# Optimization experiments

Hardware: AMD Instinct MI355X
Metric: run time of the kernel (lower is better)

Reference implementation:

```python
import jax, jax.numpy as jnp
import numpy as np
from jax import lax

D_MODEL, D_STATE, D_CONV, D_INNER, DT_RANK = 1024, 16, 4, 2048, 64
B_SZ, L_SEQ = 2, 4096

def setup_inputs() -> dict:
    key = jax.random.key(0)
    ks = jax.random.split(key, 12)
    s = 0.02
    x = jax.random.normal(ks[0], (B_SZ, L_SEQ, D_MODEL), jnp.float32)
    norm_w = jnp.ones((D_MODEL,), jnp.float32)
    norm_b = jnp.zeros((D_MODEL,), jnp.float32)
    W_in = jax.random.normal(ks[1], (D_MODEL, 2 * D_INNER), jnp.float32) * s
    conv_w = jax.random.normal(ks[2], (D_INNER, 1, D_CONV), jnp.float32) * 0.5
    conv_b = jnp.zeros((D_INNER,), jnp.float32)
    W_x = jax.random.normal(ks[3], (D_INNER, DT_RANK + 2 * D_STATE), jnp.float32) * s
    W_dt = jax.random.normal(ks[4], (DT_RANK, D_INNER), jnp.float32) * s
    # dt bias init as in the torch module: inverse-softplus of dt in [dt_min, dt_max]
    dt_init = jnp.exp(jax.random.uniform(ks[5], (D_INNER,)) * (np.log(0.1) - np.log(0.001)) + np.log(0.001))
    dt_init = jnp.clip(dt_init, 1e-4, None)
    b_dt = dt_init + jnp.log(-jnp.expm1(-dt_init))
    A_log = jnp.log(jnp.broadcast_to(jnp.arange(1, D_STATE + 1, dtype=jnp.float32)[None, :], (D_INNER, D_STATE)))
    D = jnp.ones((D_INNER,), jnp.float32)
    W_out = jax.random.normal(ks[6], (D_INNER, D_MODEL), jnp.float32) * s
    return {"x": x, "norm_w": norm_w, "norm_b": norm_b, "W_in": W_in,
            "conv_w": conv_w, "conv_b": conv_b, "W_x": W_x, "W_dt": W_dt,
            "b_dt": b_dt, "A_log": A_log, "D": D, "W_out": W_out}

def _silu(v):
    return v * jax.nn.sigmoid(v)

def _layernorm(v, w, b, eps=1e-5):
    mu = jnp.mean(v, axis=-1, keepdims=True)
    var = jnp.var(v, axis=-1, keepdims=True)
    return (v - mu) * lax.rsqrt(var + eps) * w + b

def _selective_scan(u, delta, A, Bm, Cm, Dp):
    # u, delta: [B,L,d_inner]; A: [d_inner,N]; Bm, Cm: [B,L,N]; Dp: [d_inner]
    Bb, L, d_inner = u.shape
    N = A.shape[1]

    def step(h, inp):
        dt_t, u_t, B_t, C_t = inp  # [B,d_inner],[B,d_inner],[B,N],[B,N]
        A_bar = jnp.exp(dt_t[..., None] * A)                       # [B,d_inner,N]
        h = A_bar * h + dt_t[..., None] * B_t[:, None, :] * u_t[..., None]
        y = jnp.sum(h * C_t[:, None, :], axis=-1)                  # [B,d_inner]
        return h, y

    h0 = jnp.zeros((Bb, d_inner, N), u.dtype)
    xs = (jnp.swapaxes(delta, 0, 1), jnp.swapaxes(u, 0, 1),
          jnp.swapaxes(Bm, 0, 1), jnp.swapaxes(Cm, 0, 1))
    _, ys = lax.scan(step, h0, xs)          # ys: [L,B,d_inner]
    y = jnp.swapaxes(ys, 0, 1)
    return y + u * Dp[None, None, :]

def reference(x, norm_w, norm_b, W_in, conv_w, conv_b, W_x, W_dt, b_dt, A_log, D, W_out):
    residual = x
    xn = _layernorm(x, norm_w, norm_b)
    xz = xn @ W_in                                      # [B,L,2*d_inner]
    x_ssm, z = jnp.split(xz, 2, axis=-1)
    # depthwise causal conv1d (torch pads both sides then truncates -> left pad)
    xt = jnp.swapaxes(x_ssm, 1, 2)                      # [B,d_inner,L]
    xt = jnp.pad(xt, ((0, 0), (0, 0), (D_CONV - 1, 0)))
    xc = lax.conv_general_dilated(xt, conv_w, window_strides=(1,), padding='VALID',
                                  feature_group_count=D_INNER,
                                  dimension_numbers=('NCH', 'OIH', 'NCH'))
    xc = xc + conv_b[None, :, None]
    x_conv = jnp.swapaxes(_silu(xc), 1, 2)              # [B,L,d_inner]
    x_dbl = x_conv @ W_x                                # [B,L,dt_rank+2N]
    dt_low, B_mat, C_mat = jnp.split(x_dbl, [DT_RANK, DT_RANK + D_STATE], axis=-1)
    delta = jax.nn.softplus(dt_low @ W_dt + b_dt)       # [B,L,d_inner]
    A = -jnp.exp(A_log)
    y = _selective_scan(x_conv, delta, A, B_mat, C_mat, D)
    y = y * _silu(z)
    return residual + y @ W_out
```

## Files before the change

### kernel.cpp

```cpp
#include <hip/hip_runtime.h>

typedef unsigned short u16;
typedef __attribute__((ext_vector_type(8))) __bf16 bf16x8;
typedef __attribute__((ext_vector_type(4))) float f32x4;

#define LSEQ 4096
#define DMODEL 1024
#define DINNER 2048

__device__ __forceinline__ float bf2f(u16 u) {
  union { unsigned u; float f; } v; v.u = ((unsigned)u) << 16; return v.f;
}
__device__ __forceinline__ u16 f2bf(float f) {
  union { float f; unsigned u; } v; v.f = f;
  unsigned r = v.u + 0x7fffu + ((v.u >> 16) & 1u);
  return (u16)(r >> 16);
}
__device__ __forceinline__ void gload_lds16(const void* g, void* l) {
  __builtin_amdgcn_global_load_lds(
      (__attribute__((address_space(1))) void*)(unsigned long long)g,
      (__attribute__((address_space(3))) void*)(unsigned int)(unsigned long long)l,
      16, 0, 0);
}
__device__ __forceinline__ float sigmoidf_(float v) { return 1.f / (1.f + __expf(-v)); }

__device__ __forceinline__ void swz_block(int gx, int& bn, int& bm) {
  int lin = blockIdx.x + gridDim.x * blockIdx.y;
  int q = (gridDim.x * gridDim.y) >> 3;
  int s = (lin & 7) * q + (lin >> 3);
  bn = s % gx;
  bm = s / gx;
}

__global__ __launch_bounds__(256) void ln_kernel(const float* __restrict__ x,
                                                 const float* __restrict__ w,
                                                 const float* __restrict__ b,
                                                 u16* __restrict__ out) {
  int row = blockIdx.x;
  const float* xr = x + (size_t)row * DMODEL;
  int t = threadIdx.x;
  float4 v = ((const float4*)xr)[t];
  float s = v.x + v.y + v.z + v.w;
  float s2 = v.x * v.x + v.y * v.y + v.z * v.z + v.w * v.w;
  for (int off = 32; off; off >>= 1) {
    s += __shfl_down(s, off);
    s2 += __shfl_down(s2, off);
  }
  __shared__ float ls[4], ls2[4];
  int wid = t >> 6;
  if ((t & 63) == 0) { ls[wid] = s; ls2[wid] = s2; }
  __syncthreads();
  s = ls[0] + ls[1] + ls[2] + ls[3];
  s2 = ls2[0] + ls2[1] + ls2[2] + ls2[3];
  float mu = s * (1.f / DMODEL);
  float var = s2 * (1.f / DMODEL) - mu * mu;
  float rs = rsqrtf(var + 1e-5f);
  float4 wv = ((const float4*)w)[t];
  float4 bv = ((const float4*)b)[t];
  unsigned p0 = (unsigned)f2bf((v.x - mu) * rs * wv.x + bv.x) |
                ((unsigned)f2bf((v.y - mu) * rs * wv.y + bv.y) << 16);
  unsigned p1 = (unsigned)f2bf((v.z - mu) * rs * wv.z + bv.z) |
                ((unsigned)f2bf((v.w - mu) * rs * wv.w + bv.w) << 16);
  ((uint2*)(out + (size_t)row * DMODEL))[t] = make_uint2(p0, p1);
}

__global__ __launch_bounds__(256) void tc_kernel(const float* __restrict__ in,
                                                 u16* __restrict__ out,
                                                 int K, int N, int Npad) {
  __shared__ float tile[32][33];
  int n0 = blockIdx.x * 32, k0 = blockIdx.y * 32;
  int tx = threadIdx.x & 31, ty = threadIdx.x >> 5;
  for (int i = ty; i < 32; i += 8) {
    int k = k0 + i, n = n0 + tx;
    tile[i][tx] = (k < K && n < N) ? in[(size_t)k * N + n] : 0.f;
  }
  __syncthreads();
  for (int i = ty; i < 32; i += 8) {
    int n = n0 + i, k = k0 + tx;
    if (n < Npad && k < K) out[(size_t)n * K + k] = f2bf(tile[tx][i]);
  }
}

__device__ __forceinline__ void stage8(const u16* grow0, int ld, int kcol0,
                                       u16* lds_u, int ln) {
  int rr = ln >> 3, kb = ln & 7;
  gload_lds16(grow0 + (size_t)rr * ld + kcol0 + ((kb ^ rr) << 3), lds_u);
}

#define LDA_FRAGS(mh, buf)                                                         \
  _Pragma("unroll") for (int mf = 0; mf < 4; ++mf)                                 \
  _Pragma("unroll") for (int kk = 0; kk < 2; ++kk)                                 \
    av[mf][kk] = *(const bf16x8*)(LA + (buf) * 16384 +                             \
        (wm * 128 + (mh) * 64 + mf * 16 + lr) * 64 + (((kk * 4 + lq) ^ key) << 3));

#define LDB_FRAGS(nh, buf)                                                         \
  _Pragma("unroll") for (int nf = 0; nf < 2; ++nf)                                 \
  _Pragma("unroll") for (int kk = 0; kk < 2; ++kk)                                 \
    bb[nh][nf][kk] = *(const bf16x8*)(LB + (buf) * 16384 +                         \
        (wn * 64 + (nh) * 32 + nf * 16 + lr) * 64 + (((kk * 4 + lq) ^ key) << 3));

#define MFMA_Q(mh, nh)                                                             \
  __builtin_amdgcn_s_setprio(1);                                                   \
  _Pragma("unroll") for (int mf = 0; mf < 4; ++mf)                                 \
  _Pragma("unroll") for (int nf = 0; nf < 2; ++nf)                                 \
  _Pragma("unroll") for (int kk = 0; kk < 2; ++kk)                                 \
    acc[(mh) * 4 + mf][(nh) * 2 + nf] = __builtin_amdgcn_mfma_f32_16x16x32_bf16(   \
        av[mf][kk], bb[nh][nf][kk], acc[(mh) * 4 + mf][(nh) * 2 + nf], 0, 0, 0);   \
  __builtin_amdgcn_s_setprio(0);

#define STAGE_A(unit, kt, buf)                                                     \
  _Pragma("unroll") for (int c = 0; c < 2; ++c) {                                  \
    int g = w * 2 + c;                                                             \
    int r0 = ((g < 8) ? g * 8 : (g - 8) * 8 + 128) + (unit) * 64;                  \
    stage8(Ag + (size_t)r0 * ldK, ldK, (kt) * 64, LA + (buf) * 16384 + r0 * 64, ln); \
  }

#define STAGE_B(half, kt, buf)                                                     \
  _Pragma("unroll") for (int c = 0; c < 2; ++c) {                                  \
    int g = w * 2 + c;                                                             \
    int r0 = (g >> 2) * 64 + (half) * 32 + (g & 3) * 8;                            \
    stage8(Bg + (size_t)r0 * ldK, ldK, (kt) * 64, LB + (buf) * 16384 + r0 * 64, ln); \
  }

template <int OUT_BF16, int EPI>
__global__ __launch_bounds__(512, 2) void gemm8p(const u16* __restrict__ A,
                                                 const u16* __restrict__ Bt,
                                                 void* __restrict__ Cout,
                                                 const float* __restrict__ aux,
                                                 int M, int N, int K, int cthresh) {
  __shared__ alignas(16) u16 lds[65536];
  u16* LA = lds;
  u16* LB = lds + 32768;
  int t = threadIdx.x;
  int w = t >> 6, ln = t & 63;
  int wm = w >> 2, wn = w & 3;
  int bn, bm;
  swz_block(gridDim.x, bn, bm);
  int lr = ln & 15, lq = ln >> 4, key = ln & 7;
  int ldK = K;
  int NT = K >> 6;
  const u16* Ag = A + (size_t)bm * 256 * ldK;
  const u16* Bg = Bt + (size_t)bn * 256 * ldK;
  f32x4 acc[8][4] = {};
  bf16x8 av[4][2], bb[2][2][2];

  STAGE_A(0, 0, 0); STAGE_B(0, 0, 0); STAGE_B(1, 0, 0); STAGE_A(1, 0, 0);
  int k1 = NT > 1 ? 1 : 0;
  STAGE_A(0, k1, 1); STAGE_B(0, k1, 1); STAGE_B(1, k1, 1);
  asm volatile("s_waitcnt vmcnt(6)" ::: "memory");
  __builtin_amdgcn_s_barrier();

  for (int T = 0; T < NT; ++T) {
    int b0 = T & 1, b1 = b0 ^ 1;
    int kt1 = (T + 1 < NT) ? T + 1 : NT - 1;
    int kt2 = (T + 2 < NT) ? T + 2 : NT - 1;
    LDA_FRAGS(0, b0);
    LDB_FRAGS(0, b0);
    STAGE_A(1, kt1, b1);
    __builtin_amdgcn_s_barrier();
    asm volatile("s_waitcnt lgkmcnt(0)" ::: "memory");
    MFMA_Q(0, 0);
    __builtin_amdgcn_s_barrier();
    LDB_FRAGS(1, b0);
    STAGE_A(0, kt2, b0);
    __builtin_amdgcn_s_barrier();
    asm volatile("s_waitcnt lgkmcnt(0)" ::: "memory");
    MFMA_Q(0, 1);
    __builtin_amdgcn_s_barrier();
    LDA_FRAGS(1, b0);
    STAGE_B(0, kt2, b0);
    __builtin_amdgcn_s_barrier();
    asm volatile("s_waitcnt lgkmcnt(0)" ::: "memory");
    MFMA_Q(1, 1);
    __builtin_amdgcn_s_barrier();
    STAGE_B(1, kt2, b0);
    asm volatile("s_waitcnt vmcnt(6)" ::: "memory");
    __builtin_amdgcn_s_barrier();
    MFMA_Q(1, 0);
    __builtin_amdgcn_s_barrier();
  }

  int crow0 = bm * 256 + wm * 128;
  int ccol0 = bn * 256 + wn * 64;
#pragma unroll
  for (int mf = 0; mf < 8; ++mf)
#pragma unroll
    for (int nf = 0; nf < 4; ++nf)
#pragma unroll
      for (int r = 0; r < 4; ++r) {
        int row = crow0 + mf * 16 + lq * 4 + r;
        int col = ccol0 + nf * 16 + lr;
        float v = acc[mf][nf][r];
        if (EPI == 1) v += aux[(size_t)row * N + col];
        if (EPI == 2 && col >= cthresh) v = v * sigmoidf_(v);
        if (OUT_BF16)
          ((u16*)Cout)[(size_t)row * N + col] = f2bf(v);
        else
          ((float*)Cout)[(size_t)row * N + col] = v;
      }
}

#define LDA128(mh, buf)                                                            \
  _Pragma("unroll") for (int mf2 = 0; mf2 < 2; ++mf2)                              \
  _Pragma("unroll") for (int kk = 0; kk < 2; ++kk)                                 \
    av[mf2][kk] = *(const bf16x8*)(LA + (buf) * 8192 +                             \
        (wm * 64 + (mh) * 32 + mf2 * 16 + lr) * 64 + (((kk * 4 + lq) ^ key) << 3));

#define LDB128(nh, buf, B_)                                                        \
  _Pragma("unroll") for (int nf2 = 0; nf2 < 2; ++nf2)                              \
  _Pragma("unroll") for (int kk = 0; kk < 2; ++kk)                                 \
    B_[nf2][kk] = *(const bf16x8*)(LB + (buf) * 16384 +                            \
        (wn * 64 + (nh) * 32 + nf2 * 16 + lr) * 64 + (((kk * 4 + lq) ^ key) << 3));

#define MFMA_Q128(mh, nh, B_)                                                      \
  __builtin_amdgcn_s_setprio(1);                                                   \
  _Pragma("unroll") for (int mf2 = 0; mf2 < 2; ++mf2)                              \
  _Pragma("unroll") for (int nf2 = 0; nf2 < 2; ++nf2)                              \
  _Pragma("unroll") for (int kk = 0; kk < 2; ++kk)                                 \
    acc[(mh) * 2 + mf2][(nh) * 2 + nf2] = __builtin_amdgcn_mfma_f32_16x16x32_bf16( \
        av[mf2][kk], B_[nf2][kk], acc[(mh) * 2 + mf2][(nh) * 2 + nf2], 0, 0, 0);   \
  __builtin_amdgcn_s_setprio(0);

#define STAGE_A128(unit, kt, buf)                                                  \
  {                                                                                \
    int r0 = (w >> 2) * 64 + (unit) * 32 + (w & 3) * 8;                            \
    stage8(Ag + (size_t)r0 * ldK, ldK, (kt) * 64, LA + (buf) * 8192 + r0 * 64, ln); \
  }

#define STAGE_B128(half, kt, buf)                                                  \
  _Pragma("unroll") for (int c = 0; c < 2; ++c) {                                  \
    int g = w * 2 + c;                                                             \
    int r0 = (g >> 2) * 64 + (half) * 32 + (g & 3) * 8;                            \
    stage8(Bg + (size_t)r0 * ldK, ldK, (kt) * 64, LB + (buf) * 16384 + r0 * 64, ln); \
  }

__global__ __launch_bounds__(512, 2) void gemm128_res(const u16* __restrict__ A,
                                                      const u16* __restrict__ Bt,
                                                      float* __restrict__ Cout,
                                                      const float* __restrict__ res,
                                                      int M, int N, int K) {
  __shared__ alignas(16) u16 lds[49152];
  u16* LA = lds;
  u16* LB = lds + 16384;
  int t = threadIdx.x;
  int w = t >> 6, ln = t & 63;
  int wm = w >> 2, wn = w & 3;
  int bn, bm;
  swz_block(gridDim.x, bn, bm);
  int lr = ln & 15, lq = ln >> 4, key = ln & 7;
  int ldK = K;
  int NT = K >> 6;
  const u16* Ag = A + (size_t)bm * 128 * ldK;
  const u16* Bg = Bt + (size_t)bn * 256 * ldK;
  f32x4 acc[4][4] = {};
  bf16x8 av[2][2], bbl[2][2], bbh[2][2];

  STAGE_A128(0, 0, 0); STAGE_B128(0, 0, 0); STAGE_B128(1, 0, 0); STAGE_A128(1, 0, 0);
  int k1 = NT > 1 ? 1 : 0;
  STAGE_A128(0, k1, 1); STAGE_B128(0, k1, 1); STAGE_B128(1, k1, 1);
  asm volatile("s_waitcnt vmcnt(5)" ::: "memory");
  __builtin_amdgcn_s_barrier();

  for (int T = 0; T < NT; ++T) {
    int b0 = T & 1, b1 = b0 ^ 1;
    int kt1 = (T + 1 < NT) ? T + 1 : NT - 1;
    int kt2 = (T + 2 < NT) ? T + 2 : NT - 1;
    LDA128(0, b0);
    LDB128(0, b0, bbl);
    STAGE_A128(1, kt1, b1);
    __builtin_amdgcn_s_barrier();
    asm volatile("s_waitcnt lgkmcnt(0)" ::: "memory");
    MFMA_Q128(0, 0, bbl);
    __builtin_amdgcn_s_barrier();
    LDB128(1, b0, bbh);
    STAGE_A128(0, kt2, b0);
    __builtin_amdgcn_s_barrier();
    asm volatile("s_waitcnt lgkmcnt(0)" ::: "memory");
    MFMA_Q128(0, 1, bbh);
    __builtin_amdgcn_s_barrier();
    LDA128(1, b0);
    STAGE_B128(0, kt2, b0);
    __builtin_amdgcn_s_barrier();
    asm volatile("s_waitcnt lgkmcnt(0)" ::: "memory");
    MFMA_Q128(1, 1, bbh);
    __builtin_amdgcn_s_barrier();
    STAGE_B128(1, kt2, b0);
    asm volatile("s_waitcnt vmcnt(5)" ::: "memory");
    __builtin_amdgcn_s_barrier();
    MFMA_Q128(1, 0, bbl);
    __builtin_amdgcn_s_barrier();
  }

  int crow0 = bm * 128 + wm * 64;
  int ccol0 = bn * 256 + wn * 64;
#pragma unroll
  for (int mf = 0; mf < 4; ++mf)
#pragma unroll
    for (int nf = 0; nf < 4; ++nf)
#pragma unroll
      for (int r = 0; r < 4; ++r) {
        int row = crow0 + mf * 16 + lq * 4 + r;
        int col = ccol0 + nf * 16 + lr;
        Cout[(size_t)row * N + col] = acc[mf][nf][r] + res[(size_t)row * N + col];
      }
}

template <int OUT_BF16, int EPI, int SPLITK>
__global__ __launch_bounds__(256) void gemm_bt(const u16* __restrict__ A,
                                               const u16* __restrict__ Bt,
                                               void* __restrict__ Cout,
                                               const float* __restrict__ aux,
                                               int M, int N, int K, int ld, int cthresh) {
  __shared__ alignas(16) u16 As[128 * 32];
  __shared__ alignas(16) u16 Bs[128 * 32];
  int t = threadIdx.x;
  int w = t >> 6, ln = t & 63;
  int wr = w >> 1, wc = w & 1;
  int bm = blockIdx.y, bn = blockIdx.x;
  int lr = ln & 15, lk = (ln >> 4) * 8;
  f32x4 acc[4][4] = {};
  int kz = SPLITK ? blockIdx.z * K : 0;
  const u16* Abase = A + (size_t)bm * 128 * ld + kz;
  const u16* Bbase = Bt + (size_t)bn * 128 * ld + kz;
  for (int k0 = 0; k0 < K; k0 += 32) {
#pragma unroll
    for (int c = 0; c < 2; ++c) {
      int chunk = w * 2 + c;
      int ee = chunk * 512 + ln * 8;
      int row = ee >> 5, col = ee & 31;
      gload_lds16(Abase + (size_t)row * ld + k0 + col, As + chunk * 512);
      gload_lds16(Bbase + (size_t)row * ld + k0 + col, Bs + chunk * 512);
    }
    __syncthreads();
    bf16x8 af[4], bfr[4];
#pragma unroll
    for (int m = 0; m < 4; ++m)
      af[m] = *(const bf16x8*)(As + (wr * 64 + m * 16 + lr) * 32 + lk);
#pragma unroll
    for (int n = 0; n < 4; ++n)
      bfr[n] = *(const bf16x8*)(Bs + (wc * 64 + n * 16 + lr) * 32 + lk);
#pragma unroll
    for (int m = 0; m < 4; ++m)
#pragma unroll
      for (int n = 0; n < 4; ++n)
        acc[m][n] = __builtin_amdgcn_mfma_f32_16x16x32_bf16(af[m], bfr[n], acc[m][n], 0, 0, 0);
    __syncthreads();
  }
  int rb = bm * 128 + wr * 64 + (ln >> 4) * 4;
  int cb = bn * 128 + wc * 64 + lr;
  float* Cpart = SPLITK ? ((float*)Cout + (size_t)blockIdx.z * M * N) : (float*)Cout;
#pragma unroll
  for (int m = 0; m < 4; ++m)
#pragma unroll
    for (int n = 0; n < 4; ++n)
#pragma unroll
      for (int r = 0; r < 4; ++r) {
        int row = rb + m * 16 + r;
        int col = cb + n * 16;
        float v = acc[m][n][r];
        if (EPI == 3) {
          float dtr = v + aux[col];
          v = dtr > 15.f ? dtr : __logf(1.f + __expf(dtr));
        }
        if (OUT_BF16)
          ((u16*)Cpart)[(size_t)row * N + col] = f2bf(v);
        else
          Cpart[(size_t)row * N + col] = v;
      }
}

__global__ __launch_bounds__(256) void reduce_xdbl(const float* __restrict__ part,
                                                   float* __restrict__ xdbl,
                                                   u16* __restrict__ dtlow) {
  int i = blockIdx.x * 256 + threadIdx.x;
  float s = 0.f;
#pragma unroll
  for (int z = 0; z < 8; ++z) s += part[(size_t)z * (8192 * 128) + i];
  xdbl[i] = s;
  int col = i & 127;
  if (col < 64) dtlow[(size_t)(i >> 7) * 64 + col] = f2bf(s);
}

__global__ __launch_bounds__(256) void conv_silu(const u16* __restrict__ xz,
                                                 const float* __restrict__ cw,
                                                 const float* __restrict__ cb,
                                                 u16* __restrict__ out) {
  int d = blockIdx.x * 256 + threadIdx.x;
  int l0 = blockIdx.y * 8;
  int b = blockIdx.z;
  float w0 = cw[d * 4 + 0], w1 = cw[d * 4 + 1], w2 = cw[d * 4 + 2], w3 = cw[d * 4 + 3];
  float bias = cb[d];
  const u16* xp = xz + ((size_t)b * LSEQ) * 4096 + d;
  float xv[11];
#pragma unroll
  for (int i = 0; i < 11; ++i) {
    int l = l0 - 3 + i;
    xv[i] = (l >= 0) ? bf2f(xp[(size_t)l * 4096]) : 0.f;
  }
  u16* op = out + ((size_t)b * LSEQ + l0) * DINNER + d;
#pragma unroll
  for (int i = 0; i < 8; ++i) {
    float acc = bias + w0 * xv[i] + w1 * xv[i + 1] + w2 * xv[i + 2] + w3 * xv[i + 3];
    float sv = acc * sigmoidf_(acc);
    op[(size_t)i * DINNER] = f2bf(sv);
  }
}

__device__ __forceinline__ void compute_a(float dt, const float* An, bool fast, float* av) {
  if (fast) {
    float q = __expf(-dt);
    float q2 = q * q, q4 = q2 * q2;
    av[0] = q; av[1] = q2; av[2] = q2 * q; av[3] = q4;
#pragma unroll
    for (int n = 4; n < 16; ++n) av[n] = av[n - 4] * q4;
  } else {
#pragma unroll
    for (int n = 0; n < 16; ++n) av[n] = __expf(dt * An[n]);
  }
}

__global__ __launch_bounds__(256) void scan1(const u16* __restrict__ dtbf,
                                             const u16* __restrict__ ubf,
                                             const float* __restrict__ xdbl,
                                             const float* __restrict__ A_log,
                                             float* __restrict__ P,
                                             float* __restrict__ H) {
  int d = blockIdx.x * 256 + threadIdx.x;
  int b = blockIdx.y, c = blockIdx.z;
  size_t row0 = (size_t)b * LSEQ + c * 64;
  float An[16];
  bool fast = true;
  {
    const float4* A4 = (const float4*)(A_log + (size_t)d * 16);
#pragma unroll
    for (int q = 0; q < 4; ++q) {
      float4 a = A4[q];
      An[q * 4 + 0] = -__expf(a.x);
      An[q * 4 + 1] = -__expf(a.y);
      An[q * 4 + 2] = -__expf(a.z);
      An[q * 4 + 3] = -__expf(a.w);
    }
#pragma unroll
    for (int n = 0; n < 16; ++n)
      fast = fast && (__builtin_fabsf(An[n] + (float)(n + 1)) < 1e-3f * (n + 1));
  }
  const u16* dtp = dtbf + row0 * DINNER + d;
  const u16* up = ubf + row0 * DINNER + d;
  const float* Bp = xdbl + row0 * 128 + 64;
  float h[16];
#pragma unroll
  for (int n = 0; n < 16; ++n) h[n] = 0.f;
  float sdt = 0.f;
#pragma unroll 2
  for (int i = 0; i < 64; ++i) {
    float dt = bf2f(dtp[(size_t)i * DINNER]);
    float uu = bf2f(up[(size_t)i * DINNER]);
    float dtu = dt * uu;
    sdt += dt;
    const float4* B4 = (const float4*)(Bp + (size_t)i * 128);
    float4 b0 = B4[0], b1 = B4[1], b2 = B4[2], b3 = B4[3];
    float Bf[16] = {b0.x, b0.y, b0.z, b0.w, b1.x, b1.y, b1.z, b1.w,
                    b2.x, b2.y, b2.z, b2.w, b3.x, b3.y, b3.z, b3.w};
    float av[16];
    compute_a(dt, An, fast, av);
#pragma unroll
    for (int n = 0; n < 16; ++n) h[n] = av[n] * h[n] + dtu * Bf[n];
  }
  size_t idx = (size_t)c * 65536 + ((size_t)b * DINNER + d) * 16;
  float4* P4 = (float4*)(P + idx);
  float4* H4 = (float4*)(H + idx);
#pragma unroll
  for (int q = 0; q < 4; ++q) {
    P4[q] = make_float4(__expf(An[q * 4 + 0] * sdt), __expf(An[q * 4 + 1] * sdt),
                        __expf(An[q * 4 + 2] * sdt), __expf(An[q * 4 + 3] * sdt));
    H4[q] = make_float4(h[q * 4], h[q * 4 + 1], h[q * 4 + 2], h[q * 4 + 3]);
  }
}

__global__ __launch_bounds__(256) void scan2(const float* __restrict__ P,
                                             const float* __restrict__ H,
                                             float* __restrict__ Hinit) {
  int i = blockIdx.x * 256 + threadIdx.x;
  float h = 0.f;
  for (int c = 0; c < 64; ++c) {
    Hinit[(size_t)c * 65536 + i] = h;
    h = P[(size_t)c * 65536 + i] * h + H[(size_t)c * 65536 + i];
  }
}

__global__ __launch_bounds__(256) void scan3(const u16* __restrict__ dtbf,
                                             const u16* __restrict__ ubf,
                                             const float* __restrict__ xdbl,
                                             const float* __restrict__ A_log,
                                             const float* __restrict__ Dp,
                                             const u16* __restrict__ xzbf,
                                             const float* __restrict__ Hinit,
                                             u16* __restrict__ ybf) {
  int d = blockIdx.x * 256 + threadIdx.x;
  int b = blockIdx.y, c = blockIdx.z;
  size_t row0 = (size_t)b * LSEQ + c * 64;
  float An[16];
  bool fast = true;
  {
    const float4* A4 = (const float4*)(A_log + (size_t)d * 16);
#pragma unroll
    for (int q = 0; q < 4; ++q) {
      float4 a = A4[q];
      An[q * 4 + 0] = -__expf(a.x);
      An[q * 4 + 1] = -__expf(a.y);
      An[q * 4 + 2] = -__expf(a.z);
      An[q * 4 + 3] = -__expf(a.w);
    }
#pragma unroll
    for (int n = 0; n < 16; ++n)
      fast = fast && (__builtin_fabsf(An[n] + (float)(n + 1)) < 1e-3f * (n + 1));
  }
  const u16* dtp = dtbf + row0 * DINNER + d;
  const u16* up = ubf + row0 * DINNER + d;
  const float* Bp = xdbl + row0 * 128 + 64;
  const float* Cp = xdbl + row0 * 128 + 80;
  const u16* gp = xzbf + row0 * 4096 + DINNER + d;
  u16* yp = ybf + row0 * DINNER + d;
  float Dv = Dp[d];
  float h[16];
  {
    const float4* Hi4 = (const float4*)(Hinit + (size_t)c * 65536 + ((size_t)b * DINNER + d) * 16);
#pragma unroll
    for (int q = 0; q < 4; ++q) {
      float4 hv = Hi4[q];
      h[q * 4 + 0] = hv.x; h[q * 4 + 1] = hv.y; h[q * 4 + 2] = hv.z; h[q * 4 + 3] = hv.w;
    }
  }
#pragma unroll 2
  for (int i = 0; i < 64; ++i) {
    float dt = bf2f(dtp[(size_t)i * DINNER]);
    float uu = bf2f(up[(size_t)i * DINNER]);
    float dtu = dt * uu;
    const float4* B4 = (const float4*)(Bp + (size_t)i * 128);
    float4 b0 = B4[0], b1 = B4[1], b2 = B4[2], b3 = B4[3];
    float Bf[16] = {b0.x, b0.y, b0.z, b0.w, b1.x, b1.y, b1.z, b1.w,
                    b2.x, b2.y, b2.z, b2.w, b3.x, b3.y, b3.z, b3.w};
    const float4* C4 = (const float4*)(Cp + (size_t)i * 128);
    float4 c0 = C4[0], c1 = C4[1], c2 = C4[2], c3 = C4[3];
    float Cf[16] = {c0.x, c0.y, c0.z, c0.w, c1.x, c1.y, c1.z, c1.w,
                    c2.x, c2.y, c2.z, c2.w, c3.x, c3.y, c3.z, c3.w};
    float av[16];
    compute_a(dt, An, fast, av);
    float y = 0.f;
#pragma unroll
    for (int n = 0; n < 16; ++n) {
      h[n] = av[n] * h[n] + dtu * Bf[n];
      y += h[n] * Cf[n];
    }
    float g = bf2f(gp[(size_t)i * 4096]);
    yp[(size_t)i * DINNER] = f2bf((y + uu * Dv) * g);
  }
}

extern "C" void kernel_launch(void* const* d_in, const int* in_sizes, int n_in,
                              void* d_out, int out_size, void* d_ws, size_t ws_size,
                              hipStream_t stream) {
  const float* x = (const float*)d_in[0];
  const float* nw = (const float*)d_in[1];
  const float* nb = (const float*)d_in[2];
  const float* W_in = (const float*)d_in[3];
  const float* convw = (const float*)d_in[4];
  const float* convb = (const float*)d_in[5];
  const float* W_x = (const float*)d_in[6];
  const float* W_dt = (const float*)d_in[7];
  const float* b_dt = (const float*)d_in[8];
  const float* A_log = (const float*)d_in[9];
  const float* Dp = (const float*)d_in[10];
  const float* W_out = (const float*)d_in[11];
  float* out = (float*)d_out;

  char* wp = (char*)d_ws;
  auto alloc = [&](size_t bytes) {
    char* p = wp;
    wp += (bytes + 255) & ~(size_t)255;
    return p;
  };
  u16* xz_bf = (u16*)alloc((size_t)8192 * 4096 * 2);
  u16* xconv_bf = (u16*)alloc((size_t)8192 * 2048 * 2);
  u16* xn_bf = (u16*)alloc((size_t)8192 * 1024 * 2);
  float* xdbl = (float*)alloc((size_t)8192 * 128 * 4);
  u16* dt_bf = (u16*)alloc((size_t)8192 * 2048 * 2);
  u16* dtlow_bf = (u16*)alloc((size_t)8192 * 64 * 2);
  u16* Wint = (u16*)alloc((size_t)4096 * 1024 * 2);
  u16* Wxt = (u16*)alloc((size_t)128 * 2048 * 2);
  u16* Wdtt = (u16*)alloc((size_t)2048 * 64 * 2);
  u16* Woutt = (u16*)alloc((size_t)1024 * 2048 * 2);
  float* P = (float*)alloc((size_t)64 * 65536 * 4);
  float* H = (float*)alloc((size_t)64 * 65536 * 4);
  float* Hinit = (float*)alloc((size_t)64 * 65536 * 4);
  float* xdbl_part = (float*)P;
  u16* y_bf = (u16*)P;

  tc_kernel<<<dim3(128, 32), 256, 0, stream>>>(W_in, Wint, 1024, 4096, 4096);
  tc_kernel<<<dim3(4, 64), 256, 0, stream>>>(W_x, Wxt, 2048, 96, 128);
  tc_kernel<<<dim3(64, 2), 256, 0, stream>>>(W_dt, Wdtt, 64, 2048, 2048);
  tc_kernel<<<dim3(32, 64), 256, 0, stream>>>(W_out, Woutt, 2048, 1024, 1024);

  ln_kernel<<<8192, 256, 0, stream>>>(x, nw, nb, xn_bf);
  gemm8p<1, 2><<<dim3(16, 32), 512, 0, stream>>>(xn_bf, Wint, xz_bf, nullptr,
                                                 8192, 4096, 1024, 2048);
  conv_silu<<<dim3(8, 512, 2), 256, 0, stream>>>(xz_bf, convw, convb, xconv_bf);
  gemm_bt<0, 0, 1><<<dim3(1, 64, 8), 256, 0, stream>>>(xconv_bf, Wxt, xdbl_part, nullptr,
                                                       8192, 128, 256, 2048, 0);
  reduce_xdbl<<<4096, 256, 0, stream>>>(xdbl_part, xdbl, dtlow_bf);
  gemm_bt<1, 3, 0><<<dim3(16, 64), 256, 0, stream>>>(dtlow_bf, Wdtt, dt_bf, b_dt,
                                                     8192, 2048, 64, 64, 0);
  scan1<<<dim3(8, 2, 64), 256, 0, stream>>>(dt_bf, xconv_bf, xdbl, A_log, P, H);
  scan2<<<256, 256, 0, stream>>>(P, H, Hinit);
  scan3<<<dim3(8, 2, 64), 256, 0, stream>>>(dt_bf, xconv_bf, xdbl, A_log, Dp, xz_bf,
                                            Hinit, y_bf);
  gemm128_res<<<dim3(4, 64), 512, 0, stream>>>(y_bf, Woutt, out, x, 8192, 1024, 2048);
}
```

Measured before the change: 317.4 us.

## Merge weight transposes, vectorize conv by channel pairs, prefetch scan inputs

The four weight-transpose launches become one kernel that picks its matrix from the block index, which removes launch overhead. conv_silu now handles two adjacent channels per thread using 32-bit packed loads and stores, halving the grid and the number of memory transactions. scan1 and scan3 software-pipeline their per-timestep loads, fetching step i+1's dt, u, B, C and gate values while step i computes, to hide global load latency in the serial recurrence. The prefetch raises register pressure, which could reduce occupancy.

```diff
diff --git a/kernel.cpp b/kernel.cpp
--- a/kernel.cpp
+++ b/kernel.cpp
@@ -64,11 +64,22 @@
   ((uint2*)(out + (size_t)row * DMODEL))[t] = make_uint2(p0, p1);
 }
 
-__global__ __launch_bounds__(256) void tc_kernel(const float* __restrict__ in,
-                                                 u16* __restrict__ out,
-                                                 int K, int N, int Npad) {
+__global__ __launch_bounds__(256) void tc_all(const float* __restrict__ W_in,
+                                              const float* __restrict__ W_x,
+                                              const float* __restrict__ W_dt,
+                                              const float* __restrict__ W_out,
+                                              u16* __restrict__ o0, u16* __restrict__ o1,
+                                              u16* __restrict__ o2, u16* __restrict__ o3) {
   __shared__ float tile[32][33];
-  int n0 = blockIdx.x * 32, k0 = blockIdx.y * 32;
+  int id = blockIdx.x;
+  const float* in;
+  u16* out;
+  int K, N, Npad, gx, bx;
+  if (id < 4096)      { in = W_in;  out = o0; K = 1024; N = 4096; Npad = 4096; gx = 128; bx = id; }
+  else if (id < 4352) { in = W_x;   out = o1; K = 2048; N = 96;   Npad = 128;  gx = 4;   bx = id - 4096; }
+  else if (id < 4480) { in = W_dt;  out = o2; K = 64;   N = 2048; Npad = 2048; gx = 64;  bx = id - 4352; }
+  else                { in = W_out; out = o3; K = 2048; N = 1024; Npad = 1024; gx = 32;  bx = id - 4480; }
+  int n0 = (bx % gx) * 32, k0 = (bx / gx) * 32;
   int tx = threadIdx.x & 31, ty = threadIdx.x >> 5;
   for (int i = ty; i < 32; i += 8) {
     int k = k0 + i, n = n0 + tx;
@@ -385,24 +396,30 @@
                                                  const float* __restrict__ cw,
                                                  const float* __restrict__ cb,
                                                  u16* __restrict__ out) {
-  int d = blockIdx.x * 256 + threadIdx.x;
+  int d2 = blockIdx.x * 256 + threadIdx.x;
+  int d = d2 * 2;
   int l0 = blockIdx.y * 8;
   int b = blockIdx.z;
-  float w0 = cw[d * 4 + 0], w1 = cw[d * 4 + 1], w2 = cw[d * 4 + 2], w3 = cw[d * 4 + 3];
-  float bias = cb[d];
+  float w0a = cw[d * 4 + 0], w1a = cw[d * 4 + 1], w2a = cw[d * 4 + 2], w3a = cw[d * 4 + 3];
+  float w0b = cw[d * 4 + 4], w1b = cw[d * 4 + 5], w2b = cw[d * 4 + 6], w3b = cw[d * 4 + 7];
+  float biasa = cb[d], biasb = cb[d + 1];
   const u16* xp = xz + ((size_t)b * LSEQ) * 4096 + d;
-  float xv[11];
+  float xa[11], xb[11];
 #pragma unroll
   for (int i = 0; i < 11; ++i) {
     int l = l0 - 3 + i;
-    xv[i] = (l >= 0) ? bf2f(xp[(size_t)l * 4096]) : 0.f;
+    unsigned pk = (l >= 0) ? *(const unsigned*)(xp + (size_t)l * 4096) : 0u;
+    xa[i] = bf2f((u16)(pk & 0xffffu));
+    xb[i] = bf2f((u16)(pk >> 16));
   }
   u16* op = out + ((size_t)b * LSEQ + l0) * DINNER + d;
 #pragma unroll
   for (int i = 0; i < 8; ++i) {
-    float acc = bias + w0 * xv[i] + w1 * xv[i + 1] + w2 * xv[i + 2] + w3 * xv[i + 3];
-    float sv = acc * sigmoidf_(acc);
-    op[(size_t)i * DINNER] = f2bf(sv);
+    float va = biasa + w0a * xa[i] + w1a * xa[i + 1] + w2a * xa[i + 2] + w3a * xa[i + 3];
+    float vb = biasb + w0b * xb[i] + w1b * xb[i + 1] + w2b * xb[i + 2] + w3b * xb[i + 3];
+    unsigned pk = (unsigned)f2bf(va * sigmoidf_(va)) |
+                  ((unsigned)f2bf(vb * sigmoidf_(vb)) << 16);
+    *(unsigned*)(op + (size_t)i * DINNER) = pk;
   }
 }
 
@@ -417,6 +434,22 @@
 #pragma unroll
     for (int n = 0; n < 16; ++n) av[n] = __expf(dt * An[n]);
   }
+}
+
+__device__ __forceinline__ void load_An(const float* A_log, int d, float* An, bool& fast) {
+  const float4* A4 = (const float4*)(A_log + (size_t)d * 16);
+  fast = true;
+#pragma unroll
+  for (int q = 0; q < 4; ++q) {
+    float4 a = A4[q];
+    An[q * 4 + 0] = -__expf(a.x);
+    An[q * 4 + 1] = -__expf(a.y);
+    An[q * 4 + 2] = -__expf(a.z);
+    An[q * 4 + 3] = -__expf(a.w);
+  }
+#pragma unroll
+  for (int n = 0; n < 16; ++n)
+    fast = fast && (__builtin_fabsf(An[n] + (float)(n + 1)) < 1e-3f * (n + 1));
 }
 
 __global__ __launch_bounds__(256) void scan1(const u16* __restrict__ dtbf,
@@ -429,21 +462,8 @@
   int b = blockIdx.y, c = blockIdx.z;
   size_t row0 = (size_t)b * LSEQ + c * 64;
   float An[16];
-  bool fast = true;
-  {
-    const float4* A4 = (const float4*)(A_log + (size_t)d * 16);
-#pragma unroll
-    for (int q = 0; q < 4; ++q) {
-      float4 a = A4[q];
-      An[q * 4 + 0] = -__expf(a.x);
-      An[q * 4 + 1] = -__expf(a.y);
-      An[q * 4 + 2] = -__expf(a.z);
-      An[q * 4 + 3] = -__expf(a.w);
-    }
-#pragma unroll
-    for (int n = 0; n < 16; ++n)
-      fast = fast && (__builtin_fabsf(An[n] + (float)(n + 1)) < 1e-3f * (n + 1));
-  }
+  bool fast;
+  load_An(A_log, d, An, fast);
   const u16* dtp = dtbf + row0 * DINNER + d;
   const u16* up = ubf + row0 * DINNER + d;
   const float* Bp = xdbl + row0 * 128 + 64;
@@ -451,20 +471,29 @@
 #pragma unroll
   for (int n = 0; n < 16; ++n) h[n] = 0.f;
   float sdt = 0.f;
-#pragma unroll 2
+  float dt_c = bf2f(dtp[0]);
+  float uu_c = bf2f(up[0]);
+  const float4* B4 = (const float4*)Bp;
+  float4 b0c = B4[0], b1c = B4[1], b2c = B4[2], b3c = B4[3];
   for (int i = 0; i < 64; ++i) {
-    float dt = bf2f(dtp[(size_t)i * DINNER]);
-    float uu = bf2f(up[(size_t)i * DINNER]);
-    float dtu = dt * uu;
-    sdt += dt;
-    const float4* B4 = (const float4*)(Bp + (size_t)i * 128);
-    float4 b0 = B4[0], b1 = B4[1], b2 = B4[2], b3 = B4[3];
-    float Bf[16] = {b0.x, b0.y, b0.z, b0.w, b1.x, b1.y, b1.z, b1.w,
-                    b2.x, b2.y, b2.z, b2.w, b3.x, b3.y, b3.z, b3.w};
+    float dt_n = dt_c, uu_n = uu_c;
+    float4 b0n = b0c, b1n = b1c, b2n = b2c, b3n = b3c;
+    if (i < 63) {
+      dt_n = bf2f(dtp[(size_t)(i + 1) * DINNER]);
+      uu_n = bf2f(up[(size_t)(i + 1) * DINNER]);
+      const float4* B4n = (const float4*)(Bp + (size_t)(i + 1) * 128);
+      b0n = B4n[0]; b1n = B4n[1]; b2n = B4n[2]; b3n = B4n[3];
+    }
+    float dtu = dt_c * uu_c;
+    sdt += dt_c;
+    float Bf[16] = {b0c.x, b0c.y, b0c.z, b0c.w, b1c.x, b1c.y, b1c.z, b1c.w,
+                    b2c.x, b2c.y, b2c.z, b2c.w, b3c.x, b3c.y, b3c.z, b3c.w};
     float av[16];
-    compute_a(dt, An, fast, av);
+    compute_a(dt_c, An, fast, av);
 #pragma unroll
     for (int n = 0; n < 16; ++n) h[n] = av[n] * h[n] + dtu * Bf[n];
+    dt_c = dt_n; uu_c = uu_n;
+    b0c = b0n; b1c = b1n; b2c = b2n; b3c = b3n;
   }
   size_t idx = (size_t)c * 65536 + ((size_t)b * DINNER + d) * 16;
   float4* P4 = (float4*)(P + idx);
@@ -500,21 +529,8 @@
   int b = blockIdx.y, c = blockIdx.z;
   size_t row0 = (size_t)b * LSEQ + c * 64;
   float An[16];
-  bool fast = true;
-  {
-    const float4* A4 = (const float4*)(A_log + (size_t)d * 16);
-#pragma unroll
-    for (int q = 0; q < 4; ++q) {
-      float4 a = A4[q];
-      An[q * 4 + 0] = -__expf(a.x);
-      An[q * 4 + 1] = -__expf(a.y);
-      An[q * 4 + 2] = -__expf(a.z);
-      An[q * 4 + 3] = -__expf(a.w);
-    }
-#pragma unroll
-    for (int n = 0; n < 16; ++n)
-      fast = fast && (__builtin_fabsf(An[n] + (float)(n + 1)) < 1e-3f * (n + 1));
-  }
+  bool fast;
+  load_An(A_log, d, An, fast);
   const u16* dtp = dtbf + row0 * DINNER + d;
   const u16* up = ubf + row0 * DINNER + d;
   const float* Bp = xdbl + row0 * 128 + 64;
@@ -531,29 +547,43 @@
       h[q * 4 + 0] = hv.x; h[q * 4 + 1] = hv.y; h[q * 4 + 2] = hv.z; h[q * 4 + 3] = hv.w;
     }
   }
-#pragma unroll 2
+  float dt_c = bf2f(dtp[0]);
+  float uu_c = bf2f(up[0]);
+  float g_c = bf2f(gp[0]);
+  const float4* B4 = (const float4*)Bp;
+  const float4* C4 = (const float4*)Cp;
+  float4 b0c = B4[0], b1c = B4[1], b2c = B4[2], b3c = B4[3];
+  float4 c0c = C4[0], c1c = C4[1], c2c = C4[2], c3c = C4[3];
   for (int i = 0; i < 64; ++i) {
-    float dt = bf2f(dtp[(size_t)i * DINNER]);
-    float uu = bf2f(up[(size_t)i * DINNER]);
-    float dtu = dt * uu;
-    const float4* B4 = (const float4*)(Bp + (size_t)i * 128);
-    float4 b0 = B4[0], b1 = B4[1], b2 = B4[2], b3 = B4[3];
-    float Bf[16] = {b0.x, b0.y, b0.z, b0.w, b1.x, b1.y, b1.z, b1.w,
-                    b2.x, b2.y, b2.z, b2.w, b3.x, b3.y, b3.z, b3.w};
-    const float4* C4 = (const float4*)(Cp + (size_t)i * 128);
-    float4 c0 = C4[0], c1 = C4[1], c2 = C4[2], c3 = C4[3];
-    float Cf[16] = {c0.x, c0.y, c0.z, c0.w, c1.x, c1.y, c1.z, c1.w,
-                    c2.x, c2.y, c2.z, c2.w, c3.x, c3.y, c3.z, c3.w};
+    float dt_n = dt_c, uu_n = uu_c, g_n = g_c;
+    float4 b0n = b0c, b1n = b1c, b2n = b2c, b3n = b3c;
+    float4 c0n = c0c, c1n = c1c, c2n = c2c, c3n = c3c;
+    if (i < 63) {
+      dt_n = bf2f(dtp[(size_t)(i + 1) * DINNER]);
+      uu_n = bf2f(up[(size_t)(i + 1) * DINNER]);
+      g_n = bf2f(gp[(size_t)(i + 1) * 4096]);
+      const float4* B4n = (const float4*)(Bp + (size_t)(i + 1) * 128);
+      const float4* C4n = (const float4*)(Cp + (size_t)(i + 1) * 128);
+      b0n = B4n[0]; b1n = B4n[1]; b2n = B4n[2]; b3n = B4n[3];
+      c0n = C4n[0]; c1n = C4n[1]; c2n = C4n[2]; c3n = C4n[3];
+    }
+    float dtu = dt_c * uu_c;
+    float Bf[16] = {b0c.x, b0c.y, b0c.z, b0c.w, b1c.x, b1c.y, b1c.z, b1c.w,
+                    b2c.x, b2c.y, b2c.z, b2c.w, b3c.x, b3c.y, b3c.z, b3c.w};
+    float Cf[16] = {c0c.x, c0c.y, c0c.z, c0c.w, c1c.x, c1c.y, c1c.z, c1c.w,
+                    c2c.x, c2c.y, c2c.z, c2c.w, c3c.x, c3c.y, c3c.z, c3c.w};
     float av[16];
-    compute_a(dt, An, fast, av);
+    compute_a(dt_c, An, fast, av);
     float y = 0.f;
 #pragma unroll
     for (int n = 0; n < 16; ++n) {
       h[n] = av[n] * h[n] + dtu * Bf[n];
       y += h[n] * Cf[n];
     }
-    float g = bf2f(gp[(size_t)i * 4096]);
-    yp[(size_t)i * DINNER] = f2bf((y + uu * Dv) * g);
+    yp[(size_t)i * DINNER] = f2bf((y + uu_c * Dv) * g_c);
+    dt_c = dt_n; uu_c = uu_n; g_c = g_n;
+    b0c = b0n; b1c = b1n; b2c = b2n; b3c = b3n;
+    c0c = c0n; c1c = c1n; c2c = c2n; c3c = c3n;
   }
 }
 
@@ -596,15 +626,12 @@
   float* xdbl_part = (float*)P;
   u16* y_bf = (u16*)P;
 
-  tc_kernel<<<dim3(128, 32), 256, 0, stream>>>(W_in, Wint, 1024, 4096, 4096);
-  tc_kernel<<<dim3(4, 64), 256, 0, stream>>>(W_x, Wxt, 2048, 96, 128);
-  tc_kernel<<<dim3(64, 2), 256, 0, stream>>>(W_dt, Wdtt, 64, 2048, 2048);
-  tc_kernel<<<dim3(32, 64), 256, 0, stream>>>(W_out, Woutt, 2048, 1024, 1024);
+  tc_all<<<6528, 256, 0, stream>>>(W_in, W_x, W_dt, W_out, Wint, Wxt, Wdtt, Woutt);
 
   ln_kernel<<<8192, 256, 0, stream>>>(x, nw, nb, xn_bf);
   gemm8p<1, 2><<<dim3(16, 32), 512, 0, stream>>>(xn_bf, Wint, xz_bf, nullptr,
                                                  8192, 4096, 1024, 2048);
-  conv_silu<<<dim3(8, 512, 2), 256, 0, stream>>>(xz_bf, convw, convb, xconv_bf);
+  conv_silu<<<dim3(4, 512, 2), 256, 0, stream>>>(xz_bf, convw, convb, xconv_bf);
   gemm_bt<0, 0, 1><<<dim3(1, 64, 8), 256, 0, stream>>>(xconv_bf, Wxt, xdbl_part, nullptr,
                                                        8192, 128, 256, 2048, 0);
   reduce_xdbl<<<4096, 256, 0, stream>>>(xdbl_part, xdbl, dtlow_bf);
```

Result: no change. 313.3 us (-1.3%).
